# Optimization experiments

Measured on AMD Instinct MI355X. Metric: run time of the kernel, lower is better.

Reference implementation:

```python
import jax, jax.numpy as jnp
import numpy as np

N_NODES = 50000

def _gcn_conv(x, W, b, src, dst, num_nodes):
    # PyG GCNConv: linear transform, then D^{-1/2} A_hat D^{-1/2} aggregation (A_hat has self-loops).
    xw = x @ W                                   # [N, out]
    ones = jnp.ones(src.shape[0], dtype=x.dtype)
    deg = jax.ops.segment_sum(ones, dst, num_segments=num_nodes)  # in-degree incl. self loop
    dinv = jnp.where(deg > 0, jax.lax.rsqrt(deg), 0.0)
    norm = dinv[src] * dinv[dst]                 # [E]
    msg = xw[src] * norm[:, None]                # [E, out] gather + scale
    out = jax.ops.segment_sum(msg, dst, num_segments=num_nodes)   # scatter-add
    return out + b

def _add_self_loops(edge_index, num_nodes):
    loop = jnp.arange(num_nodes, dtype=edge_index.dtype)
    src = jnp.concatenate([edge_index[0], loop])
    dst = jnp.concatenate([edge_index[1], loop])
    return src, dst

def setup_inputs() -> dict:
    key = jax.random.key(0)
    k = jax.random.split(key, 6)
    in_dim, hid_dim, out_dim = 256, 128, 64
    n_edges = 800000
    x = jax.random.normal(k[0], (N_NODES, in_dim), dtype=jnp.float32)
    edge_index = jax.random.randint(k[1], (2, n_edges), 0, N_NODES, dtype=jnp.int64)
    W1 = jax.random.normal(k[2], (in_dim, hid_dim), dtype=jnp.float32) / np.sqrt(in_dim)
    b1 = jnp.zeros((hid_dim,), dtype=jnp.float32)
    W2 = jax.random.normal(k[3], (hid_dim, out_dim), dtype=jnp.float32) / np.sqrt(hid_dim)
    b2 = jnp.zeros((out_dim,), dtype=jnp.float32)
    return {"x": x, "edge_index": edge_index, "W1": W1, "b1": b1, "W2": W2, "b2": b2}

def reference(x, edge_index, W1, b1, W2, b2):
    src, dst = _add_self_loops(edge_index, N_NODES)
    h = jnp.tanh(_gcn_conv(x, W1, b1, src, dst, N_NODES))
    out = _gcn_conv(h, W2, b2, src, dst, N_NODES)
    return out
```

## Files before the change

kernel.cpp:

```cpp
#include <hip/hip_runtime.h>

#define INDIM 256
#define HID 128
#define OUTD 64
#define BINSHIFT 8
#define MAXBIN 256

typedef _Float16 f16x8 __attribute__((ext_vector_type(8)));
typedef float    f32x4 __attribute__((ext_vector_type(4)));

__global__ __launch_bounds__(256) void k_hist_prep(const int* __restrict__ dst, int* __restrict__ hist_part,
                                                   int E,
                                                   const float* __restrict__ W1, const float* __restrict__ W2,
                                                   _Float16* __restrict__ W1t, _Float16* __restrict__ W2t) {
    __shared__ int h[MAXBIN];
    int tid = threadIdx.x;
    h[tid] = 0;
    __syncthreads();
    int base = blockIdx.x * 4096;
#pragma unroll
    for (int i = 0; i < 16; i++) {
        int e = base + i * 256 + tid;
        if (e < E) atomicAdd(&h[dst[e] >> BINSHIFT], 1);
    }
    __syncthreads();
    hist_part[blockIdx.x * MAXBIN + tid] = h[tid];

    constexpr int NW1 = HID * INDIM;
    constexpr int NW2 = OUTD * HID;
    int id = blockIdx.x * 256 + tid;
    if (id < NW1) {
        int n = id / INDIM, k = id % INDIM;
        W1t[id] = (_Float16)W1[k * HID + n];
    } else if (id < NW1 + NW2) {
        int j = id - NW1;
        int n = j / HID, k = j % HID;
        W2t[j] = (_Float16)W2[k * OUTD + n];
    }
}

__global__ __launch_bounds__(256) void k_scan(const int* __restrict__ hist_part, int NWH,
                                              int* __restrict__ bin_start, int* __restrict__ bin_cursor,
                                              int* __restrict__ row_start, int NBIN, int M, int E) {
    __shared__ int s[256];
    int tid = threadIdx.x;
    int a0 = 0, a1 = 0, a2 = 0, a3 = 0;
    int w = 0;
    for (; w + 3 < NWH; w += 4) {
        a0 += hist_part[(w + 0) * MAXBIN + tid];
        a1 += hist_part[(w + 1) * MAXBIN + tid];
        a2 += hist_part[(w + 2) * MAXBIN + tid];
        a3 += hist_part[(w + 3) * MAXBIN + tid];
    }
    for (; w < NWH; w++) a0 += hist_part[w * MAXBIN + tid];
    int v = (a0 + a1) + (a2 + a3);
    if (tid >= NBIN) v = 0;
    s[tid] = v;
    __syncthreads();
#pragma unroll
    for (int off = 1; off < 256; off <<= 1) {
        int t = (tid >= off) ? s[tid - off] : 0;
        __syncthreads();
        s[tid] += t;
        __syncthreads();
    }
    if (tid < NBIN) {
        int excl = s[tid] - v;
        bin_start[tid] = excl;
        bin_cursor[tid] = excl;
    }
    if (tid == 0) {
        bin_start[NBIN] = E;
        row_start[M] = E;
    }
}

__global__ __launch_bounds__(256) void k_binfill(const int* __restrict__ src, const int* __restrict__ dst,
                                                 int* __restrict__ bin_cursor, int* __restrict__ binned, int E) {
    __shared__ int h[MAXBIN];
    __shared__ int rb[MAXBIN];
    int tid = threadIdx.x;
    h[tid] = 0;
    __syncthreads();
    int base = blockIdx.x * 2048;
    int ep[8], eb[8], rk[8];
#pragma unroll
    for (int i = 0; i < 8; i++) {
        int e = base + i * 256 + tid;
        if (e < E) {
            int s = src[e], d = dst[e];
            ep[i] = (s << 8) | (d & 255);
            eb[i] = d >> BINSHIFT;
            rk[i] = atomicAdd(&h[eb[i]], 1);
        } else {
            eb[i] = -1;
        }
    }
    __syncthreads();
    int c = h[tid];
    if (c) rb[tid] = atomicAdd(&bin_cursor[tid], c);
    __syncthreads();
#pragma unroll
    for (int i = 0; i < 8; i++) {
        if (eb[i] >= 0) binned[rb[eb[i]] + rk[i]] = ep[i];
    }
}

__global__ __launch_bounds__(256) void k_csr(const int* __restrict__ binned, const int* __restrict__ bin_start,
                                             int* __restrict__ row_start, float* __restrict__ dinv,
                                             int* __restrict__ edge_src, int M) {
    __shared__ int cnt[256];
    __shared__ int s[256];
    __shared__ int cur[256];
    int b = blockIdx.x, tid = threadIdx.x;
    int beg = bin_start[b], end = bin_start[b + 1];
    cnt[tid] = 0;
    __syncthreads();
    for (int i = beg + tid; i < end; i += 256) {
        atomicAdd(&cnt[binned[i] & 255], 1);
    }
    __syncthreads();
    int c = cnt[tid];
    s[tid] = c;
    __syncthreads();
#pragma unroll
    for (int off = 1; off < 256; off <<= 1) {
        int t = (tid >= off) ? s[tid - off] : 0;
        __syncthreads();
        s[tid] += t;
        __syncthreads();
    }
    int start = beg + s[tid] - c;
    int node = (b << BINSHIFT) + tid;
    if (node < M) {
        row_start[node] = start;
        dinv[node] = rsqrtf(1.0f + (float)c);
    }
    cur[tid] = start;
    __syncthreads();
    for (int i = beg + tid; i < end; i += 256) {
        int p = binned[i];
        int pos = atomicAdd(&cur[p & 255], 1);
        edge_src[pos] = p >> 8;
    }
}

template <int BN, int K, typename AT>
__global__ __launch_bounds__(256) void k_gemm_mfma(
    const AT* __restrict__ X, const _Float16* __restrict__ Wt,
    const float* __restrict__ dinv, _Float16* __restrict__ XW16, int M)
{
    constexpr int BM = 64;
    constexpr int BK = 32;
    constexpr int NT = BN / 16;
    constexpr int LDK = BK + 8;

    __shared__ __align__(16) _Float16 As[BM][LDK];
    __shared__ __align__(16) _Float16 Bs[BN][LDK];

    const int tid  = threadIdx.x;
    const int wave = tid >> 6;
    const int lane = tid & 63;
    const int m    = lane & 15;
    const int q    = lane >> 4;
    const int rb   = blockIdx.x * BM;

    f32x4 acc[NT];
#pragma unroll
    for (int t = 0; t < NT; t++) acc[t] = (f32x4){0.f, 0.f, 0.f, 0.f};

    for (int kt = 0; kt < K; kt += BK) {
        if (kt) __syncthreads();
        if constexpr (sizeof(AT) == 4) {
#pragma unroll
            for (int i = 0; i < BM * 8 / 256; i++) {
                int ch  = tid + i * 256;
                int row = ch >> 3;
                int c4  = ch & 7;
                int gr  = rb + row;
                float4 v = make_float4(0.f, 0.f, 0.f, 0.f);
                if (gr < M) v = *(const float4*)((const float*)X + (long)gr * K + kt + c4 * 4);
                _Float16* p = &As[row][c4 * 4];
                p[0] = (_Float16)v.x; p[1] = (_Float16)v.y;
                p[2] = (_Float16)v.z; p[3] = (_Float16)v.w;
            }
        } else {
            int row = tid >> 2;
            int c8  = tid & 3;
            int gr  = rb + row;
            uint4 v = make_uint4(0u, 0u, 0u, 0u);
            if (gr < M) v = *(const uint4*)((const _Float16*)X + (long)gr * K + kt + c8 * 8);
            *(uint4*)(&As[row][c8 * 8]) = v;
        }
#pragma unroll
        for (int i = 0; i < BN * 8 / 256; i++) {
            int ch = tid + i * 256;
            int n  = ch >> 3;
            int c4 = ch & 7;
            *(ushort4*)(&Bs[n][c4 * 4]) =
                *(const ushort4*)(Wt + (long)n * K + kt + c4 * 4);
        }
        __syncthreads();

        f16x8 af = *(const f16x8*)(&As[wave * 16 + m][q * 8]);
#pragma unroll
        for (int t = 0; t < NT; t++) {
            f16x8 bf = *(const f16x8*)(&Bs[t * 16 + m][q * 8]);
            acc[t] = __builtin_amdgcn_mfma_f32_16x16x32_f16(af, bf, acc[t], 0, 0, 0);
        }
    }

    int row0 = rb + wave * 16 + q * 4;
#pragma unroll
    for (int r = 0; r < 4; r++) {
        int row = row0 + r;
        if (row < M) {
            float di = dinv[row];
#pragma unroll
            for (int t = 0; t < NT; t++) {
                XW16[(long)row * BN + t * 16 + m] = (_Float16)(acc[t][r] * di);
            }
        }
    }
}

template <int F, bool TANH, typename OutT>
__global__ __launch_bounds__(256) void k_agg_csr(const int* __restrict__ row_start,
                                                 const int* __restrict__ edge_src,
                                                 const _Float16* __restrict__ feat,
                                                 const float* __restrict__ bias,
                                                 const float* __restrict__ dinv,
                                                 OutT* __restrict__ out, int M) {
    constexpr int LPN = F / 8;
    constexpr int NPB = 256 / LPN;
    int n = blockIdx.x * NPB + threadIdx.x / LPN;
    int c = threadIdx.x % LPN;
    if (n >= M) return;
    int beg = row_start[n], end = row_start[n + 1];

    f16x8 self = *(const f16x8*)(feat + (long)n * F + c * 8);
    float a0[8], a1[8], a2[8], a3[8];
#pragma unroll
    for (int k = 0; k < 8; k++) { a0[k] = (float)self[k]; a1[k] = 0.f; a2[k] = 0.f; a3[k] = 0.f; }

    int j = beg;
    for (; j + 7 < end; j += 8) {
        int s0 = edge_src[j],     s1 = edge_src[j + 1];
        int s2 = edge_src[j + 2], s3 = edge_src[j + 3];
        int s4 = edge_src[j + 4], s5 = edge_src[j + 5];
        int s6 = edge_src[j + 6], s7 = edge_src[j + 7];
        f16x8 v0 = *(const f16x8*)(feat + (long)s0 * F + c * 8);
        f16x8 v1 = *(const f16x8*)(feat + (long)s1 * F + c * 8);
        f16x8 v2 = *(const f16x8*)(feat + (long)s2 * F + c * 8);
        f16x8 v3 = *(const f16x8*)(feat + (long)s3 * F + c * 8);
        f16x8 v4 = *(const f16x8*)(feat + (long)s4 * F + c * 8);
        f16x8 v5 = *(const f16x8*)(feat + (long)s5 * F + c * 8);
        f16x8 v6 = *(const f16x8*)(feat + (long)s6 * F + c * 8);
        f16x8 v7 = *(const f16x8*)(feat + (long)s7 * F + c * 8);
#pragma unroll
        for (int k = 0; k < 8; k++) {
            a0[k] += (float)v0[k] + (float)v1[k];
            a1[k] += (float)v2[k] + (float)v3[k];
            a2[k] += (float)v4[k] + (float)v5[k];
            a3[k] += (float)v6[k] + (float)v7[k];
        }
    }
    for (; j + 3 < end; j += 4) {
        int s0 = edge_src[j],     s1 = edge_src[j + 1];
        int s2 = edge_src[j + 2], s3 = edge_src[j + 3];
        f16x8 v0 = *(const f16x8*)(feat + (long)s0 * F + c * 8);
        f16x8 v1 = *(const f16x8*)(feat + (long)s1 * F + c * 8);
        f16x8 v2 = *(const f16x8*)(feat + (long)s2 * F + c * 8);
        f16x8 v3 = *(const f16x8*)(feat + (long)s3 * F + c * 8);
#pragma unroll
        for (int k = 0; k < 8; k++) {
            a0[k] += (float)v0[k] + (float)v1[k];
            a1[k] += (float)v2[k] + (float)v3[k];
        }
    }
    for (; j < end; j++) {
        int s = edge_src[j];
        f16x8 v = *(const f16x8*)(feat + (long)s * F + c * 8);
#pragma unroll
        for (int k = 0; k < 8; k++) a0[k] += (float)v[k];
    }

    float di = dinv[n];
    float acc[8];
#pragma unroll
    for (int k = 0; k < 8; k++)
        acc[k] = bias[c * 8 + k] + di * ((a0[k] + a1[k]) + (a2[k] + a3[k]));
    if (TANH) {
#pragma unroll
        for (int k = 0; k < 8; k++) acc[k] = tanhf(acc[k]);
    }
    if constexpr (sizeof(OutT) == 2) {
        f16x8 o;
#pragma unroll
        for (int k = 0; k < 8; k++) o[k] = (_Float16)acc[k];
        __builtin_nontemporal_store(o, (f16x8*)((_Float16*)out + (long)n * F + c * 8));
    } else {
        f32x4 o0 = {acc[0], acc[1], acc[2], acc[3]};
        f32x4 o1 = {acc[4], acc[5], acc[6], acc[7]};
        float* p = (float*)out + (long)n * F + c * 8;
        __builtin_nontemporal_store(o0, (f32x4*)p);
        __builtin_nontemporal_store(o1, (f32x4*)(p + 4));
    }
}

extern "C" void kernel_launch(void* const* d_in, const int* in_sizes, int n_in,
                              void* d_out, int out_size, void* d_ws, size_t ws_size,
                              hipStream_t stream) {
    const float* x  = (const float*)d_in[0];
    const int*   ei = (const int*)d_in[1];
    const float* W1 = (const float*)d_in[2];
    const float* b1 = (const float*)d_in[3];
    const float* W2 = (const float*)d_in[4];
    const float* b2 = (const float*)d_in[5];
    float* out = (float*)d_out;

    const int M = in_sizes[0] / INDIM;
    const int E = in_sizes[1] / 2;
    const int* srcp = ei;
    const int* dstp = ei + E;

    const int Mp   = (M + 63) & ~63;
    const int NBIN = (M + 255) >> BINSHIFT;
    int NWH = (E + 4095) / 4096;
    if (NWH < 161) NWH = 161;
    const int NWF = (E + 2047) / 2048;

    float*     dinv       = (float*)d_ws;
    int*       row_start  = (int*)(dinv + Mp);
    int*       bin_start  = row_start + Mp;
    int*       bin_cursor = bin_start + 258;
    int*       hist_part  = bin_cursor + MAXBIN;
    _Float16*  W1t        = (_Float16*)(hist_part + (long)NWH * MAXBIN);
    _Float16*  W2t        = W1t + HID * INDIM;
    int*       binned     = (int*)(W2t + OUTD * HID);
    int*       edge_src   = binned + E;
    _Float16*  xw16       = (_Float16*)(edge_src + E);
    _Float16*  h16        = xw16 + (long)M * HID;
    _Float16*  hw16       = xw16;

    k_hist_prep<<<NWH, 256, 0, stream>>>(dstp, hist_part, E, W1, W2, W1t, W2t);
    k_scan<<<1, 256, 0, stream>>>(hist_part, NWH, bin_start, bin_cursor, row_start, NBIN, M, E);
    k_binfill<<<NWF, 256, 0, stream>>>(srcp, dstp, bin_cursor, binned, E);
    k_csr<<<NBIN, 256, 0, stream>>>(binned, bin_start, row_start, dinv, edge_src, M);

    k_gemm_mfma<HID, INDIM, float><<<(M + 63) / 64, 256, 0, stream>>>(x, W1t, dinv, xw16, M);
    k_agg_csr<HID, true, _Float16><<<(M + 15) / 16, 256, 0, stream>>>(row_start, edge_src, xw16, b1, dinv, h16, M);

    k_gemm_mfma<OUTD, HID, _Float16><<<(M + 63) / 64, 256, 0, stream>>>(h16, W2t, dinv, hw16, M);
    k_agg_csr<OUTD, false, float><<<(M + 31) / 32, 256, 0, stream>>>(row_start, edge_src, hw16, b2, dinv, out, M);
}
```

Baseline: 231.8 us.

## Store features in 16-column chunk-major layout for cache-local gather aggregation

The GEMM now writes its fp16 output in a chunk-major layout of 16-column slabs, [chunk][node][16], and the second GEMM reads its input in that layout. Aggregation becomes a per-chunk kernel in which consecutive blocks cover one column slab, so the randomly gathered rows of a slab (about 1.6 MB) can stay resident in L2. This is meant to cut the DRAM traffic of the random neighbour gathers. In exchange the adjacency list is read once per chunk, unroll depth drops from 8 to 4, and each gather is only 16 bytes wide.

```diff
diff --git a/kernel.cpp b/kernel.cpp
--- a/kernel.cpp
+++ b/kernel.cpp
@@ -188,8 +188,10 @@
             int row = tid >> 2;
             int c8  = tid & 3;
             int gr  = rb + row;
+            int kk  = kt + c8 * 8;
             uint4 v = make_uint4(0u, 0u, 0u, 0u);
-            if (gr < M) v = *(const uint4*)((const _Float16*)X + (long)gr * K + kt + c8 * 8);
+            if (gr < M)
+                v = *(const uint4*)((const _Float16*)X + ((long)(kk >> 4) * M + gr) * 16 + (kk & 15));
             *(uint4*)(&As[row][c8 * 8]) = v;
         }
 #pragma unroll
@@ -218,69 +220,49 @@
             float di = dinv[row];
 #pragma unroll
             for (int t = 0; t < NT; t++) {
-                XW16[(long)row * BN + t * 16 + m] = (_Float16)(acc[t][r] * di);
+                XW16[((long)t * M + row) * 16 + m] = (_Float16)(acc[t][r] * di);
             }
         }
     }
 }
 
-template <int F, bool TANH, typename OutT>
-__global__ __launch_bounds__(256) void k_agg_csr(const int* __restrict__ row_start,
-                                                 const int* __restrict__ edge_src,
-                                                 const _Float16* __restrict__ feat,
-                                                 const float* __restrict__ bias,
-                                                 const float* __restrict__ dinv,
-                                                 OutT* __restrict__ out, int M) {
-    constexpr int LPN = F / 8;
-    constexpr int NPB = 256 / LPN;
-    int n = blockIdx.x * NPB + threadIdx.x / LPN;
-    int c = threadIdx.x % LPN;
+template <int NC, bool TANH, typename OutT>
+__global__ __launch_bounds__(256) void k_agg_chunk(const int* __restrict__ row_start,
+                                                   const int* __restrict__ edge_src,
+                                                   const _Float16* __restrict__ feat,
+                                                   const float* __restrict__ bias,
+                                                   const float* __restrict__ dinv,
+                                                   OutT* __restrict__ out, int M) {
+    const int c  = blockIdx.x % NC;
+    const int nb = blockIdx.x / NC;
+    const int n  = nb * 128 + (threadIdx.x >> 1);
+    const int hh = threadIdx.x & 1;
     if (n >= M) return;
+    const _Float16* featc = feat + (long)c * M * 16;
+
     int beg = row_start[n], end = row_start[n + 1];
-
-    f16x8 self = *(const f16x8*)(feat + (long)n * F + c * 8);
-    float a0[8], a1[8], a2[8], a3[8];
-#pragma unroll
-    for (int k = 0; k < 8; k++) { a0[k] = (float)self[k]; a1[k] = 0.f; a2[k] = 0.f; a3[k] = 0.f; }
+    f16x8 self = *(const f16x8*)(featc + (long)n * 16 + hh * 8);
+    float a0[8], a1[8];
+#pragma unroll
+    for (int k = 0; k < 8; k++) { a0[k] = (float)self[k]; a1[k] = 0.f; }
 
     int j = beg;
-    for (; j + 7 < end; j += 8) {
+    for (; j + 3 < end; j += 4) {
         int s0 = edge_src[j],     s1 = edge_src[j + 1];
         int s2 = edge_src[j + 2], s3 = edge_src[j + 3];
-        int s4 = edge_src[j + 4], s5 = edge_src[j + 5];
-        int s6 = edge_src[j + 6], s7 = edge_src[j + 7];
-        f16x8 v0 = *(const f16x8*)(feat + (long)s0 * F + c * 8);
-        f16x8 v1 = *(const f16x8*)(feat + (long)s1 * F + c * 8);
-        f16x8 v2 = *(const f16x8*)(feat + (long)s2 * F + c * 8);
-        f16x8 v3 = *(const f16x8*)(feat + (long)s3 * F + c * 8);
-        f16x8 v4 = *(const f16x8*)(feat + (long)s4 * F + c * 8);
-        f16x8 v5 = *(const f16x8*)(feat + (long)s5 * F + c * 8);
-        f16x8 v6 = *(const f16x8*)(feat + (long)s6 * F + c * 8);
-        f16x8 v7 = *(const f16x8*)(feat + (long)s7 * F + c * 8);
+        f16x8 v0 = *(const f16x8*)(featc + (long)s0 * 16 + hh * 8);
+        f16x8 v1 = *(const f16x8*)(featc + (long)s1 * 16 + hh * 8);
+        f16x8 v2 = *(const f16x8*)(featc + (long)s2 * 16 + hh * 8);
+        f16x8 v3 = *(const f16x8*)(featc + (long)s3 * 16 + hh * 8);
 #pragma unroll
         for (int k = 0; k < 8; k++) {
             a0[k] += (float)v0[k] + (float)v1[k];
             a1[k] += (float)v2[k] + (float)v3[k];
-            a2[k] += (float)v4[k] + (float)v5[k];
-            a3[k] += (float)v6[k] + (float)v7[k];
-        }
-    }
-    for (; j + 3 < end; j += 4) {
-        int s0 = edge_src[j],     s1 = edge_src[j + 1];
-        int s2 = edge_src[j + 2], s3 = edge_src[j + 3];
-        f16x8 v0 = *(const f16x8*)(feat + (long)s0 * F + c * 8);
-        f16x8 v1 = *(const f16x8*)(feat + (long)s1 * F + c * 8);
-        f16x8 v2 = *(const f16x8*)(feat + (long)s2 * F + c * 8);
-        f16x8 v3 = *(const f16x8*)(feat + (long)s3 * F + c * 8);
-#pragma unroll
-        for (int k = 0; k < 8; k++) {
-            a0[k] += (float)v0[k] + (float)v1[k];
-            a1[k] += (float)v2[k] + (float)v3[k];
         }
     }
     for (; j < end; j++) {
         int s = edge_src[j];
-        f16x8 v = *(const f16x8*)(feat + (long)s * F + c * 8);
+        f16x8 v = *(const f16x8*)(featc + (long)s * 16 + hh * 8);
 #pragma unroll
         for (int k = 0; k < 8; k++) a0[k] += (float)v[k];
     }
@@ -288,8 +270,7 @@
     float di = dinv[n];
     float acc[8];
 #pragma unroll
-    for (int k = 0; k < 8; k++)
-        acc[k] = bias[c * 8 + k] + di * ((a0[k] + a1[k]) + (a2[k] + a3[k]));
+    for (int k = 0; k < 8; k++) acc[k] = bias[c * 16 + hh * 8 + k] + di * (a0[k] + a1[k]);
     if (TANH) {
 #pragma unroll
         for (int k = 0; k < 8; k++) acc[k] = tanhf(acc[k]);
@@ -298,11 +279,11 @@
         f16x8 o;
 #pragma unroll
         for (int k = 0; k < 8; k++) o[k] = (_Float16)acc[k];
-        __builtin_nontemporal_store(o, (f16x8*)((_Float16*)out + (long)n * F + c * 8));
+        *(f16x8*)((_Float16*)out + ((long)c * M + n) * 16 + hh * 8) = o;
     } else {
         f32x4 o0 = {acc[0], acc[1], acc[2], acc[3]};
         f32x4 o1 = {acc[4], acc[5], acc[6], acc[7]};
-        float* p = (float*)out + (long)n * F + c * 8;
+        float* p = (float*)out + (long)n * OUTD + c * 16 + hh * 8;
         __builtin_nontemporal_store(o0, (f32x4*)p);
         __builtin_nontemporal_store(o1, (f32x4*)(p + 4));
     }
@@ -348,9 +329,11 @@
     k_binfill<<<NWF, 256, 0, stream>>>(srcp, dstp, bin_cursor, binned, E);
     k_csr<<<NBIN, 256, 0, stream>>>(binned, bin_start, row_start, dinv, edge_src, M);
 
+    const int NB128 = (M + 127) / 128;
+
     k_gemm_mfma<HID, INDIM, float><<<(M + 63) / 64, 256, 0, stream>>>(x, W1t, dinv, xw16, M);
-    k_agg_csr<HID, true, _Float16><<<(M + 15) / 16, 256, 0, stream>>>(row_start, edge_src, xw16, b1, dinv, h16, M);
+    k_agg_chunk<8, true, _Float16><<<NB128 * 8, 256, 0, stream>>>(row_start, edge_src, xw16, b1, dinv, h16, M);
 
     k_gemm_mfma<OUTD, HID, _Float16><<<(M + 63) / 64, 256, 0, stream>>>(h16, W2t, dinv, hw16, M);
-    k_agg_csr<OUTD, false, float><<<(M + 31) / 32, 256, 0, stream>>>(row_start, edge_src, hw16, b2, dinv, out, M);
-}
+    k_agg_chunk<4, false, float><<<NB128 * 4, 256, 0, stream>>>(row_start, edge_src, hw16, b2, dinv, out, M);
+}
```

Result: slower. 247.3 us (+6.7%).

## Sort nodes by degree within each bin to balance aggregation wavefronts

Applied to the files above, without the earlier changes.

The CSR build kernel now does a counting sort of the nodes in each 256-node bin by in-degree (capped at 127) and writes a permutation. Both aggregation kernels visit nodes in that order, so nodes of similar degree share a wavefront and fewer lanes sit idle. The 8-wide unrolled gather loop is also dropped to cut register pressure. In exchange there are extra shared-memory scans and syncs in k_csr, one more indirection per node, and scattered output writes.

```diff
diff --git a/kernel.cpp b/kernel.cpp
--- a/kernel.cpp
+++ b/kernel.cpp
@@ -108,10 +108,11 @@
 
 __global__ __launch_bounds__(256) void k_csr(const int* __restrict__ binned, const int* __restrict__ bin_start,
                                              int* __restrict__ row_start, float* __restrict__ dinv,
-                                             int* __restrict__ edge_src, int M) {
+                                             int* __restrict__ edge_src, int* __restrict__ perm, int M) {
     __shared__ int cnt[256];
     __shared__ int s[256];
     __shared__ int cur[256];
+    __shared__ int dcur[128];
     int b = blockIdx.x, tid = threadIdx.x;
     int beg = bin_start[b], end = bin_start[b + 1];
     cnt[tid] = 0;
@@ -132,12 +133,37 @@
     }
     int start = beg + s[tid] - c;
     int node = (b << BINSHIFT) + tid;
-    if (node < M) {
+    bool valid = node < M;
+    if (valid) {
         row_start[node] = start;
         dinv[node] = rsqrtf(1.0f + (float)c);
     }
     cur[tid] = start;
-    __syncthreads();
+
+    int key = c < 127 ? c : 127;
+    __syncthreads();
+    s[tid] = 0;
+    __syncthreads();
+    if (valid) atomicAdd(&s[key], 1);
+    __syncthreads();
+    int dv = s[tid];
+    __syncthreads();
+    s[tid] = dv;
+    __syncthreads();
+#pragma unroll
+    for (int off = 1; off < 256; off <<= 1) {
+        int t = (tid >= off) ? s[tid - off] : 0;
+        __syncthreads();
+        s[tid] += t;
+        __syncthreads();
+    }
+    if (tid < 128) dcur[tid] = s[tid] - dv;
+    __syncthreads();
+    if (valid) {
+        int r = atomicAdd(&dcur[key], 1);
+        perm[(b << BINSHIFT) + r] = node;
+    }
+
     for (int i = beg + tid; i < end; i += 256) {
         int p = binned[i];
         int pos = atomicAdd(&cur[p & 255], 1);
@@ -227,44 +253,25 @@
 template <int F, bool TANH, typename OutT>
 __global__ __launch_bounds__(256) void k_agg_csr(const int* __restrict__ row_start,
                                                  const int* __restrict__ edge_src,
+                                                 const int* __restrict__ perm,
                                                  const _Float16* __restrict__ feat,
                                                  const float* __restrict__ bias,
                                                  const float* __restrict__ dinv,
                                                  OutT* __restrict__ out, int M) {
     constexpr int LPN = F / 8;
     constexpr int NPB = 256 / LPN;
-    int n = blockIdx.x * NPB + threadIdx.x / LPN;
+    int n_idx = blockIdx.x * NPB + threadIdx.x / LPN;
     int c = threadIdx.x % LPN;
-    if (n >= M) return;
+    if (n_idx >= M) return;
+    int n = perm[n_idx];
     int beg = row_start[n], end = row_start[n + 1];
 
     f16x8 self = *(const f16x8*)(feat + (long)n * F + c * 8);
-    float a0[8], a1[8], a2[8], a3[8];
-#pragma unroll
-    for (int k = 0; k < 8; k++) { a0[k] = (float)self[k]; a1[k] = 0.f; a2[k] = 0.f; a3[k] = 0.f; }
+    float a0[8], a1[8];
+#pragma unroll
+    for (int k = 0; k < 8; k++) { a0[k] = (float)self[k]; a1[k] = 0.f; }
 
     int j = beg;
-    for (; j + 7 < end; j += 8) {
-        int s0 = edge_src[j],     s1 = edge_src[j + 1];
-        int s2 = edge_src[j + 2], s3 = edge_src[j + 3];
-        int s4 = edge_src[j + 4], s5 = edge_src[j + 5];
-        int s6 = edge_src[j + 6], s7 = edge_src[j + 7];
-        f16x8 v0 = *(const f16x8*)(feat + (long)s0 * F + c * 8);
-        f16x8 v1 = *(const f16x8*)(feat + (long)s1 * F + c * 8);
-        f16x8 v2 = *(const f16x8*)(feat + (long)s2 * F + c * 8);
-        f16x8 v3 = *(const f16x8*)(feat + (long)s3 * F + c * 8);
-        f16x8 v4 = *(const f16x8*)(feat + (long)s4 * F + c * 8);
-        f16x8 v5 = *(const f16x8*)(feat + (long)s5 * F + c * 8);
-        f16x8 v6 = *(const f16x8*)(feat + (long)s6 * F + c * 8);
-        f16x8 v7 = *(const f16x8*)(feat + (long)s7 * F + c * 8);
-#pragma unroll
-        for (int k = 0; k < 8; k++) {
-            a0[k] += (float)v0[k] + (float)v1[k];
-            a1[k] += (float)v2[k] + (float)v3[k];
-            a2[k] += (float)v4[k] + (float)v5[k];
-            a3[k] += (float)v6[k] + (float)v7[k];
-        }
-    }
     for (; j + 3 < end; j += 4) {
         int s0 = edge_src[j],     s1 = edge_src[j + 1];
         int s2 = edge_src[j + 2], s3 = edge_src[j + 3];
@@ -288,8 +295,7 @@
     float di = dinv[n];
     float acc[8];
 #pragma unroll
-    for (int k = 0; k < 8; k++)
-        acc[k] = bias[c * 8 + k] + di * ((a0[k] + a1[k]) + (a2[k] + a3[k]));
+    for (int k = 0; k < 8; k++) acc[k] = bias[c * 8 + k] + di * (a0[k] + a1[k]);
     if (TANH) {
 #pragma unroll
         for (int k = 0; k < 8; k++) acc[k] = tanhf(acc[k]);
@@ -332,7 +338,8 @@
 
     float*     dinv       = (float*)d_ws;
     int*       row_start  = (int*)(dinv + Mp);
-    int*       bin_start  = row_start + Mp;
+    int*       perm       = row_start + Mp;
+    int*       bin_start  = perm + Mp;
     int*       bin_cursor = bin_start + 258;
     int*       hist_part  = bin_cursor + MAXBIN;
     _Float16*  W1t        = (_Float16*)(hist_part + (long)NWH * MAXBIN);
@@ -346,11 +353,11 @@
     k_hist_prep<<<NWH, 256, 0, stream>>>(dstp, hist_part, E, W1, W2, W1t, W2t);
     k_scan<<<1, 256, 0, stream>>>(hist_part, NWH, bin_start, bin_cursor, row_start, NBIN, M, E);
     k_binfill<<<NWF, 256, 0, stream>>>(srcp, dstp, bin_cursor, binned, E);
-    k_csr<<<NBIN, 256, 0, stream>>>(binned, bin_start, row_start, dinv, edge_src, M);
+    k_csr<<<NBIN, 256, 0, stream>>>(binned, bin_start, row_start, dinv, edge_src, perm, M);
 
     k_gemm_mfma<HID, INDIM, float><<<(M + 63) / 64, 256, 0, stream>>>(x, W1t, dinv, xw16, M);
-    k_agg_csr<HID, true, _Float16><<<(M + 15) / 16, 256, 0, stream>>>(row_start, edge_src, xw16, b1, dinv, h16, M);
+    k_agg_csr<HID, true, _Float16><<<(M + 15) / 16, 256, 0, stream>>>(row_start, edge_src, perm, xw16, b1, dinv, h16, M);
 
     k_gemm_mfma<OUTD, HID, _Float16><<<(M + 63) / 64, 256, 0, stream>>>(h16, W2t, dinv, hw16, M);
-    k_agg_csr<OUTD, false, float><<<(M + 31) / 32, 256, 0, stream>>>(row_start, edge_src, hw16, b2, dinv, out, M);
-}
+    k_agg_csr<OUTD, false, float><<<(M + 31) / 32, 256, 0, stream>>>(row_start, edge_src, perm, hw16, b2, dinv, out, M);
+}
```

Measured after the change: 246.2 us. 6.2% more time.
